# Optimization experiments

Hardware: AMD Instinct MI355X
Metric: run time of the kernel (lower is better)

Reference implementation:

```python
import jax, jax.numpy as jnp
import numpy as np


def gcn_conv(h, src, dst, n, W, b):
    # PyG GCNConv: linear, add self-loops, symmetric norm, scatter-sum, bias
    h = h @ W
    loop = jnp.arange(n)
    s = jnp.concatenate([src, loop])
    d = jnp.concatenate([dst, loop])
    deg = jax.ops.segment_sum(jnp.ones_like(d, h.dtype), d, num_segments=n)
    dinv = jnp.where(deg > 0, jax.lax.rsqrt(deg), 0.0)
    norm = dinv[s] * dinv[d]  # [E+N]
    out = jax.ops.segment_sum(h[s] * norm[:, None], d, num_segments=n)
    return out + b


def setup_inputs() -> dict:
    key = jax.random.key(0)
    ks = jax.random.split(key, 4)
    N, E, F_IN, F_H, F_OUT = 10000, 320000, 512, 128, 40
    x = jax.random.normal(ks[0], (N, F_IN), dtype=jnp.float32)
    edge_index = jax.random.randint(ks[1], (2, E), 0, N, dtype=jnp.int64)
    W1 = jax.random.normal(ks[2], (F_IN, F_H), dtype=jnp.float32) * (1.0 / np.sqrt(F_IN))
    b1 = jnp.zeros((F_H,), jnp.float32)
    W2 = jax.random.normal(ks[3], (F_H, F_OUT), dtype=jnp.float32) * (1.0 / np.sqrt(F_H))
    b2 = jnp.zeros((F_OUT,), jnp.float32)
    return {"x": x, "edge_index": edge_index, "W1": W1, "b1": b1, "W2": W2, "b2": b2}


def reference(x, edge_index, W1, b1, W2, b2):
    n = x.shape[0]
    src, dst = edge_index[0], edge_index[1]
    h = jax.nn.relu(gcn_conv(x, src, dst, n, W1, b1))
    logits = gcn_conv(h, src, dst, n, W2, b2)
    # regularizer: dense adjacency from edge list (duplicates summed), trace(L @ L)
    A = jnp.zeros((n, n), jnp.float32).at[src, dst].add(1.0)
    reg_loss = jnp.sum(A * A.T)  # == trace(A @ A)
    return jax.nn.log_softmax(logits, axis=1), reg_loss
```

## Files before the change

### kernel.cpp

```cpp
#include <hip/hip_runtime.h>
#include <hip/hip_bf16.h>


#define CAP 128

typedef __attribute__((ext_vector_type(8))) short short8;
typedef __attribute__((ext_vector_type(4))) float float4v;

__device__ __forceinline__ unsigned short f2bf(float f) {
    __hip_bfloat16 b = __float2bfloat16(f);
    return *reinterpret_cast<unsigned short*>(&b);
}
__device__ __forceinline__ float bf2f(unsigned short u) {
    __hip_bfloat16 b = *reinterpret_cast<__hip_bfloat16*>(&u);
    return __bfloat162float(b);
}

__global__ void k_prep(const float* __restrict__ W1, unsigned short* __restrict__ Bh1,
                       unsigned short* __restrict__ Bl1,
                       const float* __restrict__ W2, unsigned short* __restrict__ Bh2,
                       unsigned short* __restrict__ Bl2,
                       int* __restrict__ zbase, int zints, int p1B, int p2B) {
    int b = blockIdx.x;
    if (b < p1B) {
        int t = b * 256 + threadIdx.x;
        int lane = t & 63;
        int f = (t >> 6) % 8;
        int kb = (t >> 6) / 8;
        int kbase = kb * 32 + (lane >> 4) * 8;
        int n = f * 16 + (lane & 15);
        unsigned short hj[8], lj[8];
#pragma unroll
        for (int j = 0; j < 8; j++) {
            float v = W1[(size_t)(kbase + j) * 128 + n];
            unsigned short hb = f2bf(v);
            hj[j] = hb;
            lj[j] = f2bf(v - bf2f(hb));
        }
        ushort4 h0 = {hj[0], hj[1], hj[2], hj[3]}, h1 = {hj[4], hj[5], hj[6], hj[7]};
        ushort4 l0 = {lj[0], lj[1], lj[2], lj[3]}, l1 = {lj[4], lj[5], lj[6], lj[7]};
        ((ushort4*)Bh1)[t * 2] = h0; ((ushort4*)Bh1)[t * 2 + 1] = h1;
        ((ushort4*)Bl1)[t * 2] = l0; ((ushort4*)Bl1)[t * 2 + 1] = l1;
        return;
    }
    b -= p1B;
    if (b < p2B) {
        int t = b * 256 + threadIdx.x;
        if (t >= 4 * 3 * 64) return;
        int lane = t & 63;
        int f = (t >> 6) % 3;
        int kb = (t >> 6) / 3;
        int kbase = kb * 32 + (lane >> 4) * 8;
        int n = f * 16 + (lane & 15);
        unsigned short hj[8], lj[8];
#pragma unroll
        for (int j = 0; j < 8; j++) {
            float v = (n < 40) ? W2[(size_t)(kbase + j) * 40 + n] : 0.f;
            unsigned short hb = f2bf(v);
            hj[j] = hb;
            lj[j] = f2bf(v - bf2f(hb));
        }
        ushort4 h0 = {hj[0], hj[1], hj[2], hj[3]}, h1 = {hj[4], hj[5], hj[6], hj[7]};
        ushort4 l0 = {lj[0], lj[1], lj[2], lj[3]}, l1 = {lj[4], lj[5], lj[6], lj[7]};
        ((ushort4*)Bh2)[t * 2] = h0; ((ushort4*)Bh2)[t * 2 + 1] = h1;
        ((ushort4*)Bl2)[t * 2] = l0; ((ushort4*)Bl2)[t * 2 + 1] = l1;
        return;
    }
    b -= p2B;
    {
        int i = b * 256 + threadIdx.x;
        if (i < zints) zbase[i] = 0;
    }
}

__global__ void k_conv_fill(const float* __restrict__ x, unsigned short* __restrict__ xh,
                            int total4,
                            const int* __restrict__ src, const int* __restrict__ dst, int E,
                            int* __restrict__ cnt, unsigned short* __restrict__ csr,
                            int convB) {
    if ((int)blockIdx.x < convB) {
        int i = blockIdx.x * 256 + threadIdx.x;
        if (i < total4) {
            float4 v = ((const float4*)x)[i];
            ushort4 h;
            h.x = f2bf(v.x); h.y = f2bf(v.y); h.z = f2bf(v.z); h.w = f2bf(v.w);
            ((ushort4*)xh)[i] = h;
        }
        return;
    }
    int e = ((int)blockIdx.x - convB) * 256 + (int)threadIdx.x;
    if (e >= E) return;
    int d = dst[e];
    int pos = atomicAdd(&cnt[d], 1);
    if (pos < CAP) csr[(size_t)d * CAP + pos] = (unsigned short)src[e];
}

template <int NF, int KB>
__global__ void k_gemm1(const unsigned short* __restrict__ Xh,
                        const unsigned short* __restrict__ Bh,
                        const unsigned short* __restrict__ Bl,
                        unsigned short* __restrict__ H0, int M,
                        const int* __restrict__ cnt) {
    const int K = KB * 32, N = NF * 16;
    const int CH = NF * 64;
    __shared__ uint4 sB[2][2 * NF * 64];
    int w = threadIdx.x >> 6, lane = threadIdx.x & 63;
    int m0 = blockIdx.x * 32 + w * 16;
    bool valid = (m0 < M);
    int arow = valid ? (m0 + (lane & 15)) : 0;

    const uint4* GH = (const uint4*)Bh;
    const uint4* GL = (const uint4*)Bl;
    float4v acc[NF] = {};
    const short8* A = (const short8*)(Xh + (size_t)arow * K) + (lane >> 4);
    short8 a = A[0];

#pragma unroll
    for (int c = threadIdx.x; c < CH; c += 128) {
        sB[0][c] = GH[c];
        sB[0][CH + c] = GL[c];
    }
    __syncthreads();

    for (int kb = 0; kb < KB; kb++) {
        int slot = kb & 1;
        if (kb + 1 < KB) {
            const uint4* gh = GH + (kb + 1) * CH;
            const uint4* gl = GL + (kb + 1) * CH;
#pragma unroll
            for (int c = threadIdx.x; c < CH; c += 128) {
                sB[slot ^ 1][c] = gh[c];
                sB[slot ^ 1][CH + c] = gl[c];
            }
        }
        short8 an = (kb + 1 < KB) ? A[(kb + 1) * 4] : a;
        const short8* sb = (const short8*)sB[slot];
#pragma unroll
        for (int f = 0; f < NF; f++) {
            short8 bh = sb[f * 64 + lane];
            short8 bl = sb[CH + f * 64 + lane];
            acc[f] = __builtin_amdgcn_mfma_f32_16x16x32_bf16(a, bh, acc[f], 0, 0, 0);
            acc[f] = __builtin_amdgcn_mfma_f32_16x16x32_bf16(a, bl, acc[f], 0, 0, 0);
        }
        a = an;
        __syncthreads();
    }
    if (!valid) return;
    int row = (lane >> 4) * 4, col = lane & 15;
    float dd[4];
#pragma unroll
    for (int r = 0; r < 4; r++)
        dd[r] = rsqrtf((float)min(cnt[m0 + row + r], CAP) + 1.0f);
#pragma unroll
    for (int f = 0; f < NF; f++)
#pragma unroll
        for (int r = 0; r < 4; r++)
            H0[(size_t)(m0 + row + r) * N + f * 16 + col] = f2bf(acc[f][r] * dd[r]);
}

template <int NF, int KB>
__global__ void k_mfma_gemm2(const unsigned short* __restrict__ Ab,
                             const unsigned short* __restrict__ Bh,
                             const unsigned short* __restrict__ Bl,
                             unsigned short* __restrict__ LGb, int M,
                             const int* __restrict__ cnt) {
    const int K = KB * 32, N = NF * 16;
    const int TOT = KB * NF * 64;
    __shared__ uint4 sB[2 * KB * NF * 64];
#pragma unroll
    for (int c = threadIdx.x; c < TOT; c += 256) {
        sB[c] = ((const uint4*)Bh)[c];
        sB[TOT + c] = ((const uint4*)Bl)[c];
    }
    __syncthreads();
    int w = threadIdx.x >> 6, lane = threadIdx.x & 63;
    int m0 = blockIdx.x * 64 + w * 16;
    if (m0 >= M) return;
    float4v acc[NF] = {};
    const short8* A = (const short8*)(Ab + (size_t)(m0 + (lane & 15)) * K) + (lane >> 4);
    const short8* sb = (const short8*)sB;
#pragma unroll
    for (int kb = 0; kb < KB; kb++) {
        short8 a = A[kb * 4];
#pragma unroll
        for (int f = 0; f < NF; f++) {
            short8 bh = sb[(kb * NF + f) * 64 + lane];
            short8 bl = sb[TOT + (kb * NF + f) * 64 + lane];
            acc[f] = __builtin_amdgcn_mfma_f32_16x16x32_bf16(a, bh, acc[f], 0, 0, 0);
            acc[f] = __builtin_amdgcn_mfma_f32_16x16x32_bf16(a, bl, acc[f], 0, 0, 0);
        }
    }
    int row = (lane >> 4) * 4, col = lane & 15;
    float dd[4];
#pragma unroll
    for (int r = 0; r < 4; r++)
        dd[r] = rsqrtf((float)min(cnt[m0 + row + r], CAP) + 1.0f);
#pragma unroll
    for (int f = 0; f < NF; f++)
#pragma unroll
        for (int r = 0; r < 4; r++)
            LGb[(size_t)(m0 + row + r) * N + f * 16 + col] = f2bf(acc[f][r] * dd[r]);
}

__global__ void k_agg1_reg(const int* __restrict__ cnt, const unsigned short* __restrict__ csr,
                           const unsigned short* __restrict__ H, const float* __restrict__ b1,
                           unsigned* __restrict__ aggb,
                           const int* __restrict__ src, const int* __restrict__ dst, int E,
                           float* __restrict__ regp, int Nn, int aggBlocks) {
    if ((int)blockIdx.x < aggBlocks) {
        int wid = blockIdx.x * 4 + (threadIdx.x >> 6);
        int lane = threadIdx.x & 63;
        if (wid >= Nn) return;
        int len = min(cnt[wid], CAP);
        const unsigned* H2 = (const unsigned*)H;
        unsigned ph = H2[(unsigned)(wid << 6) + lane];
        float accx = __uint_as_float(ph << 16);
        float accy = __uint_as_float(ph & 0xffff0000u);
        const unsigned short* row = csr + (size_t)wid * CAP;
        int j = 0;
        for (; j + 16 <= len; j += 16) {
            uint4 iv0 = *(const uint4*)(row + j);
            uint4 iv1 = *(const uint4*)(row + j + 8);
            unsigned s[16];
            s[0] = iv0.x & 0xffff; s[1] = iv0.x >> 16; s[2] = iv0.y & 0xffff; s[3] = iv0.y >> 16;
            s[4] = iv0.z & 0xffff; s[5] = iv0.z >> 16; s[6] = iv0.w & 0xffff; s[7] = iv0.w >> 16;
            s[8] = iv1.x & 0xffff; s[9] = iv1.x >> 16; s[10] = iv1.y & 0xffff; s[11] = iv1.y >> 16;
            s[12] = iv1.z & 0xffff; s[13] = iv1.z >> 16; s[14] = iv1.w & 0xffff; s[15] = iv1.w >> 16;
            unsigned p[16];
#pragma unroll
            for (int q = 0; q < 16; q++) p[q] = H2[(s[q] << 6) + lane];
#pragma unroll
            for (int q = 0; q < 16; q++) {
                accx += __uint_as_float(p[q] << 16);
                accy += __uint_as_float(p[q] & 0xffff0000u);
            }
        }
        for (; j + 8 <= len; j += 8) {
            uint4 iv0 = *(const uint4*)(row + j);
            unsigned s[8];
            s[0] = iv0.x & 0xffff; s[1] = iv0.x >> 16; s[2] = iv0.y & 0xffff; s[3] = iv0.y >> 16;
            s[4] = iv0.z & 0xffff; s[5] = iv0.z >> 16; s[6] = iv0.w & 0xffff; s[7] = iv0.w >> 16;
            unsigned p[8];
#pragma unroll
            for (int q = 0; q < 8; q++) p[q] = H2[(s[q] << 6) + lane];
#pragma unroll
            for (int q = 0; q < 8; q++) {
                accx += __uint_as_float(p[q] << 16);
                accy += __uint_as_float(p[q] & 0xffff0000u);
            }
        }
        for (; j < len; j++) {
            unsigned p0 = H2[((unsigned)row[j] << 6) + lane];
            accx += __uint_as_float(p0 << 16);
            accy += __uint_as_float(p0 & 0xffff0000u);
        }
        float dd = rsqrtf((float)len + 1.0f);
        float2 bb = ((const float2*)b1)[lane];
        float vx = dd * accx + bb.x, vy = dd * accy + bb.y;
        vx = vx > 0.f ? vx : 0.f;
        vy = vy > 0.f ? vy : 0.f;
        aggb[(unsigned)(wid << 6) + lane] = (unsigned)f2bf(vx) | ((unsigned)f2bf(vy) << 16);
    } else {
        int e = ((int)blockIdx.x - aggBlocks) * 256 + (int)threadIdx.x;
        int c = 0;
        if (e < E) {
            int s = src[e];
            unsigned d = (unsigned)dst[e];
            int len = min(cnt[s], CAP);
            const unsigned short* row = csr + (size_t)s * CAP;
            for (int i = 0; i < len; i += 8) {
                uint4 v = *(const uint4*)(row + i);
                c += ((v.x & 0xffffu) == d) ? 1 : 0;
                c += ((v.x >> 16) == d && i + 1 < len) ? 1 : 0;
                c += ((v.y & 0xffffu) == d && i + 2 < len) ? 1 : 0;
                c += ((v.y >> 16) == d && i + 3 < len) ? 1 : 0;
                c += ((v.z & 0xffffu) == d && i + 4 < len) ? 1 : 0;
                c += ((v.z >> 16) == d && i + 5 < len) ? 1 : 0;
                c += ((v.w & 0xffffu) == d && i + 6 < len) ? 1 : 0;
                c += ((v.w >> 16) == d && i + 7 < len) ? 1 : 0;
            }
        }
#pragma unroll
        for (int off = 32; off; off >>= 1) c += __shfl_xor(c, off, 64);
        if ((threadIdx.x & 63) == 0 && c) atomicAdd(regp, (float)c);
    }
}

__global__ void k_agg2_lsm(const int* __restrict__ cnt, const unsigned short* __restrict__ csr,
                           const unsigned short* __restrict__ LGb, const float* __restrict__ b2,
                           const float* __restrict__ regp, float* __restrict__ out,
                           int Nn, int F) {
    int wid = (blockIdx.x * blockDim.x + threadIdx.x) >> 6;
    int lane = threadIdx.x & 63;
    if (wid >= Nn) return;
    int len = min(cnt[wid], CAP);
    bool act = lane < F;
    unsigned base = (unsigned)wid * 48 + lane;
    float acc = act ? bf2f(LGb[base]) : 0.f;
    const unsigned short* row = csr + (size_t)wid * CAP;
    int j = 0;
    for (; j + 8 <= len; j += 8) {
        uint4 idv = *(const uint4*)(row + j);
        unsigned s[8];
        s[0] = idv.x & 0xffff; s[1] = idv.x >> 16; s[2] = idv.y & 0xffff; s[3] = idv.y >> 16;
        s[4] = idv.z & 0xffff; s[5] = idv.z >> 16; s[6] = idv.w & 0xffff; s[7] = idv.w >> 16;
        unsigned short a[8];
#pragma unroll
        for (int q = 0; q < 8; q++) a[q] = act ? LGb[s[q] * 48 + lane] : (unsigned short)0;
#pragma unroll
        for (int q = 0; q < 8; q++) acc += __uint_as_float((unsigned)a[q] << 16);
    }
    for (; j < len; j++) {
        unsigned short a0 = act ? LGb[(unsigned)row[j] * 48 + lane] : (unsigned short)0;
        acc += __uint_as_float((unsigned)a0 << 16);
    }
    float dd = rsqrtf((float)len + 1.0f);
    float v = act ? dd * acc + b2[lane] : -1e30f;
    float m = v;
#pragma unroll
    for (int off = 32; off; off >>= 1) m = fmaxf(m, __shfl_xor(m, off, 64));
    float ex = act ? expf(v - m) : 0.f;
    float ssum = ex;
#pragma unroll
    for (int off = 32; off; off >>= 1) ssum += __shfl_xor(ssum, off, 64);
    if (act) out[(size_t)wid * F + lane] = v - m - logf(ssum);
    if (wid == 0 && lane == 0) out[(size_t)Nn * F] = regp[0];
}

extern "C" void kernel_launch(void* const* d_in, const int* in_sizes, int n_in,
                              void* d_out, int out_size, void* d_ws, size_t ws_size,
                              hipStream_t stream) {
    const float* x  = (const float*)d_in[0];
    const int*   ei = (const int*)d_in[1];
    const float* W1 = (const float*)d_in[2];
    const float* b1 = (const float*)d_in[3];
    const float* W2 = (const float*)d_in[4];
    const float* b2 = (const float*)d_in[5];
    float* out = (float*)d_out;

    const int FH   = in_sizes[3];
    const int FOUT = in_sizes[5];
    const int FIN  = in_sizes[2] / FH;
    const int Nn   = in_sizes[0] / FIN;
    const int E    = in_sizes[1] / 2;
    const int* src = ei;
    const int* dst = ei + E;

    int*   cnt  = (int*)d_ws;
    float* regp = (float*)(cnt + Nn);
    unsigned short* csr   = (unsigned short*)(regp + 16);
    unsigned short* Xh    = csr + (size_t)Nn * CAP;
    unsigned short* H0b   = Xh + (size_t)Nn * FIN;
    unsigned short* AGG1b = H0b + (size_t)Nn * FH;
    unsigned short* Bh1   = AGG1b + (size_t)Nn * FH;
    unsigned short* Bl1   = Bh1 + 65536;
    unsigned short* Bh2   = Bl1 + 65536;
    unsigned short* Bl2   = Bh2 + 6144;
    unsigned short* LGb   = Bl2 + 6144;

    int p1B = (16 * 8 * 64) / 256;
    int p2B = (4 * 3 * 64 + 255) / 256;
    int zints = Nn + 16;
    int zB = (zints + 255) / 256;
    k_prep<<<p1B + p2B + zB, 256, 0, stream>>>(W1, Bh1, Bl1, W2, Bh2, Bl2,
                                               cnt, zints, p1B, p2B);

    int total4 = Nn * FIN / 4;
    int convB = (total4 + 255) / 256;
    int fillB = (E + 255) / 256;
    k_conv_fill<<<convB + fillB, 256, 0, stream>>>(x, Xh, total4, src, dst, E, cnt, csr, convB);

    k_gemm1<8, 16><<<(Nn + 31) / 32, 128, 0, stream>>>(Xh, Bh1, Bl1, H0b, Nn, cnt);

    int aggBlocks = (Nn + 3) / 4;
    int regBlocks = (E + 255) / 256;
    k_agg1_reg<<<aggBlocks + regBlocks, 256, 0, stream>>>(
        cnt, csr, H0b, b1, (unsigned*)AGG1b, src, dst, E, regp, Nn, aggBlocks);

    k_mfma_gemm2<3, 4><<<(Nn + 63) / 64, 256, 0, stream>>>(AGG1b, Bh2, Bl2, LGb, Nn, cnt);

    k_agg2_lsm<<<(Nn * 64 + 255) / 256, 256, 0, stream>>>(
        cnt, csr, LGb, b2, regp, out, Nn, FOUT);
}
```

Measured before the change: 194.2 us.

## Move regularizer count into GEMM1 launch and split it across four lanes

The trace(A·A^T) edge-count work moves out of the aggregation kernel and into extra blocks of the first GEMM launch, so it can overlap with the compute-bound matmul instead of the memory-bound gather. The count loop is also restructured: four threads now scan each edge's CSR row with strided 8-element chunks, which shortens per-thread serial loops and balances load. Aggregation becomes a standalone kernel. The risk is that the extra blocks contend with GEMM blocks for CUs and may delay the GEMM tail.

```diff
diff --git a/kernel.cpp b/kernel.cpp
--- a/kernel.cpp
+++ b/kernel.cpp
@@ -96,11 +96,45 @@
 }
 
 template <int NF, int KB>
-__global__ void k_gemm1(const unsigned short* __restrict__ Xh,
-                        const unsigned short* __restrict__ Bh,
-                        const unsigned short* __restrict__ Bl,
-                        unsigned short* __restrict__ H0, int M,
-                        const int* __restrict__ cnt) {
+__global__ void k_gemm1_reg(const unsigned short* __restrict__ Xh,
+                            const unsigned short* __restrict__ Bh,
+                            const unsigned short* __restrict__ Bl,
+                            unsigned short* __restrict__ H0, int M,
+                            const int* __restrict__ cnt,
+                            const int* __restrict__ src, const int* __restrict__ dst, int E,
+                            const unsigned short* __restrict__ csr,
+                            float* __restrict__ regp, int gemmBlocks) {
+    if ((int)blockIdx.x >= gemmBlocks) {
+        int b = (int)blockIdx.x - gemmBlocks;
+        int g = threadIdx.x >> 2;
+        int sub = threadIdx.x & 3;
+        int base = b * 512;
+        int c = 0;
+        for (int it = 0; it < 16; it++) {
+            int e = base + it * 32 + g;
+            if (e < E) {
+                int s = src[e];
+                unsigned d = (unsigned)dst[e];
+                int len = min(cnt[s], CAP);
+                const unsigned short* row = csr + (size_t)s * CAP;
+                for (int i = sub * 8; i < len; i += 32) {
+                    uint4 v = *(const uint4*)(row + i);
+                    c += ((v.x & 0xffffu) == d) ? 1 : 0;
+                    c += ((v.x >> 16) == d && i + 1 < len) ? 1 : 0;
+                    c += ((v.y & 0xffffu) == d && i + 2 < len) ? 1 : 0;
+                    c += ((v.y >> 16) == d && i + 3 < len) ? 1 : 0;
+                    c += ((v.z & 0xffffu) == d && i + 4 < len) ? 1 : 0;
+                    c += ((v.z >> 16) == d && i + 5 < len) ? 1 : 0;
+                    c += ((v.w & 0xffffu) == d && i + 6 < len) ? 1 : 0;
+                    c += ((v.w >> 16) == d && i + 7 < len) ? 1 : 0;
+                }
+            }
+        }
+#pragma unroll
+        for (int off = 32; off; off >>= 1) c += __shfl_xor(c, off, 64);
+        if ((threadIdx.x & 63) == 0 && c) atomicAdd(regp, (float)c);
+        return;
+    }
     const int K = KB * 32, N = NF * 16;
     const int CH = NF * 64;
     __shared__ uint4 sB[2][2 * NF * 64];
@@ -156,6 +190,63 @@
 #pragma unroll
         for (int r = 0; r < 4; r++)
             H0[(size_t)(m0 + row + r) * N + f * 16 + col] = f2bf(acc[f][r] * dd[r]);
+}
+
+__global__ void k_agg1(const int* __restrict__ cnt, const unsigned short* __restrict__ csr,
+                       const unsigned short* __restrict__ H, const float* __restrict__ b1,
+                       unsigned* __restrict__ aggb, int Nn) {
+    int wid = (int)(blockIdx.x * blockDim.x + threadIdx.x) >> 6;
+    int lane = threadIdx.x & 63;
+    if (wid >= Nn) return;
+    int len = min(cnt[wid], CAP);
+    const unsigned* H2 = (const unsigned*)H;
+    unsigned ph = H2[(unsigned)(wid << 6) + lane];
+    float accx = __uint_as_float(ph << 16);
+    float accy = __uint_as_float(ph & 0xffff0000u);
+    const unsigned short* row = csr + (size_t)wid * CAP;
+    int j = 0;
+    for (; j + 16 <= len; j += 16) {
+        uint4 iv0 = *(const uint4*)(row + j);
+        uint4 iv1 = *(const uint4*)(row + j + 8);
+        unsigned s[16];
+        s[0] = iv0.x & 0xffff; s[1] = iv0.x >> 16; s[2] = iv0.y & 0xffff; s[3] = iv0.y >> 16;
+        s[4] = iv0.z & 0xffff; s[5] = iv0.z >> 16; s[6] = iv0.w & 0xffff; s[7] = iv0.w >> 16;
+        s[8] = iv1.x & 0xffff; s[9] = iv1.x >> 16; s[10] = iv1.y & 0xffff; s[11] = iv1.y >> 16;
+        s[12] = iv1.z & 0xffff; s[13] = iv1.z >> 16; s[14] = iv1.w & 0xffff; s[15] = iv1.w >> 16;
+        unsigned p[16];
+#pragma unroll
+        for (int q = 0; q < 16; q++) p[q] = H2[(s[q] << 6) + lane];
+#pragma unroll
+        for (int q = 0; q < 16; q++) {
+            accx += __uint_as_float(p[q] << 16);
+            accy += __uint_as_float(p[q] & 0xffff0000u);
+        }
+    }
+    for (; j + 8 <= len; j += 8) {
+        uint4 iv0 = *(const uint4*)(row + j);
+        unsigned s[8];
+        s[0] = iv0.x & 0xffff; s[1] = iv0.x >> 16; s[2] = iv0.y & 0xffff; s[3] = iv0.y >> 16;
+        s[4] = iv0.z & 0xffff; s[5] = iv0.z >> 16; s[6] = iv0.w & 0xffff; s[7] = iv0.w >> 16;
+        unsigned p[8];
+#pragma unroll
+        for (int q = 0; q < 8; q++) p[q] = H2[(s[q] << 6) + lane];
+#pragma unroll
+        for (int q = 0; q < 8; q++) {
+            accx += __uint_as_float(p[q] << 16);
+            accy += __uint_as_float(p[q] & 0xffff0000u);
+        }
+    }
+    for (; j < len; j++) {
+        unsigned p0 = H2[((unsigned)row[j] << 6) + lane];
+        accx += __uint_as_float(p0 << 16);
+        accy += __uint_as_float(p0 & 0xffff0000u);
+    }
+    float dd = rsqrtf((float)len + 1.0f);
+    float2 bb = ((const float2*)b1)[lane];
+    float vx = dd * accx + bb.x, vy = dd * accy + bb.y;
+    vx = vx > 0.f ? vx : 0.f;
+    vy = vy > 0.f ? vy : 0.f;
+    aggb[(unsigned)(wid << 6) + lane] = (unsigned)f2bf(vx) | ((unsigned)f2bf(vy) << 16);
 }
 
 template <int NF, int KB>
@@ -202,101 +293,16 @@
             LGb[(size_t)(m0 + row + r) * N + f * 16 + col] = f2bf(acc[f][r] * dd[r]);
 }
 
-__global__ void k_agg1_reg(const int* __restrict__ cnt, const unsigned short* __restrict__ csr,
-                           const unsigned short* __restrict__ H, const float* __restrict__ b1,
-                           unsigned* __restrict__ aggb,
-                           const int* __restrict__ src, const int* __restrict__ dst, int E,
-                           float* __restrict__ regp, int Nn, int aggBlocks) {
-    if ((int)blockIdx.x < aggBlocks) {
-        int wid = blockIdx.x * 4 + (threadIdx.x >> 6);
-        int lane = threadIdx.x & 63;
-        if (wid >= Nn) return;
-        int len = min(cnt[wid], CAP);
-        const unsigned* H2 = (const unsigned*)H;
-        unsigned ph = H2[(unsigned)(wid << 6) + lane];
-        float accx = __uint_as_float(ph << 16);
-        float accy = __uint_as_float(ph & 0xffff0000u);
-        const unsigned short* row = csr + (size_t)wid * CAP;
-        int j = 0;
-        for (; j + 16 <= len; j += 16) {
-            uint4 iv0 = *(const uint4*)(row + j);
-            uint4 iv1 = *(const uint4*)(row + j + 8);
-            unsigned s[16];
-            s[0] = iv0.x & 0xffff; s[1] = iv0.x >> 16; s[2] = iv0.y & 0xffff; s[3] = iv0.y >> 16;
-            s[4] = iv0.z & 0xffff; s[5] = iv0.z >> 16; s[6] = iv0.w & 0xffff; s[7] = iv0.w >> 16;
-            s[8] = iv1.x & 0xffff; s[9] = iv1.x >> 16; s[10] = iv1.y & 0xffff; s[11] = iv1.y >> 16;
-            s[12] = iv1.z & 0xffff; s[13] = iv1.z >> 16; s[14] = iv1.w & 0xffff; s[15] = iv1.w >> 16;
-            unsigned p[16];
-#pragma unroll
-            for (int q = 0; q < 16; q++) p[q] = H2[(s[q] << 6) + lane];
-#pragma unroll
-            for (int q = 0; q < 16; q++) {
-                accx += __uint_as_float(p[q] << 16);
-                accy += __uint_as_float(p[q] & 0xffff0000u);
-            }
-        }
-        for (; j + 8 <= len; j += 8) {
-            uint4 iv0 = *(const uint4*)(row + j);
-            unsigned s[8];
-            s[0] = iv0.x & 0xffff; s[1] = iv0.x >> 16; s[2] = iv0.y & 0xffff; s[3] = iv0.y >> 16;
-            s[4] = iv0.z & 0xffff; s[5] = iv0.z >> 16; s[6] = iv0.w & 0xffff; s[7] = iv0.w >> 16;
-            unsigned p[8];
-#pragma unroll
-            for (int q = 0; q < 8; q++) p[q] = H2[(s[q] << 6) + lane];
-#pragma unroll
-            for (int q = 0; q < 8; q++) {
-                accx += __uint_as_float(p[q] << 16);
-                accy += __uint_as_float(p[q] & 0xffff0000u);
-            }
-        }
-        for (; j < len; j++) {
-            unsigned p0 = H2[((unsigned)row[j] << 6) + lane];
-            accx += __uint_as_float(p0 << 16);
-            accy += __uint_as_float(p0 & 0xffff0000u);
-        }
-        float dd = rsqrtf((float)len + 1.0f);
-        float2 bb = ((const float2*)b1)[lane];
-        float vx = dd * accx + bb.x, vy = dd * accy + bb.y;
-        vx = vx > 0.f ? vx : 0.f;
-        vy = vy > 0.f ? vy : 0.f;
-        aggb[(unsigned)(wid << 6) + lane] = (unsigned)f2bf(vx) | ((unsigned)f2bf(vy) << 16);
-    } else {
-        int e = ((int)blockIdx.x - aggBlocks) * 256 + (int)threadIdx.x;
-        int c = 0;
-        if (e < E) {
-            int s = src[e];
-            unsigned d = (unsigned)dst[e];
-            int len = min(cnt[s], CAP);
-            const unsigned short* row = csr + (size_t)s * CAP;
-            for (int i = 0; i < len; i += 8) {
-                uint4 v = *(const uint4*)(row + i);
-                c += ((v.x & 0xffffu) == d) ? 1 : 0;
-                c += ((v.x >> 16) == d && i + 1 < len) ? 1 : 0;
-                c += ((v.y & 0xffffu) == d && i + 2 < len) ? 1 : 0;
-                c += ((v.y >> 16) == d && i + 3 < len) ? 1 : 0;
-                c += ((v.z & 0xffffu) == d && i + 4 < len) ? 1 : 0;
-                c += ((v.z >> 16) == d && i + 5 < len) ? 1 : 0;
-                c += ((v.w & 0xffffu) == d && i + 6 < len) ? 1 : 0;
-                c += ((v.w >> 16) == d && i + 7 < len) ? 1 : 0;
-            }
-        }
-#pragma unroll
-        for (int off = 32; off; off >>= 1) c += __shfl_xor(c, off, 64);
-        if ((threadIdx.x & 63) == 0 && c) atomicAdd(regp, (float)c);
-    }
-}
-
 __global__ void k_agg2_lsm(const int* __restrict__ cnt, const unsigned short* __restrict__ csr,
                            const unsigned short* __restrict__ LGb, const float* __restrict__ b2,
                            const float* __restrict__ regp, float* __restrict__ out,
                            int Nn, int F) {
-    int wid = (blockIdx.x * blockDim.x + threadIdx.x) >> 6;
+    int wid = (int)(blockIdx.x * blockDim.x + threadIdx.x) >> 6;
     int lane = threadIdx.x & 63;
     if (wid >= Nn) return;
     int len = min(cnt[wid], CAP);
     bool act = lane < F;
-    unsigned base = (unsigned)wid * 48 + lane;
-    float acc = act ? bf2f(LGb[base]) : 0.f;
+    float acc = act ? bf2f(LGb[(unsigned)wid * 48 + lane]) : 0.f;
     const unsigned short* row = csr + (size_t)wid * CAP;
     int j = 0;
     for (; j + 8 <= len; j += 8) {
@@ -370,12 +376,12 @@
     int fillB = (E + 255) / 256;
     k_conv_fill<<<convB + fillB, 256, 0, stream>>>(x, Xh, total4, src, dst, E, cnt, csr, convB);
 
-    k_gemm1<8, 16><<<(Nn + 31) / 32, 128, 0, stream>>>(Xh, Bh1, Bl1, H0b, Nn, cnt);
-
-    int aggBlocks = (Nn + 3) / 4;
-    int regBlocks = (E + 255) / 256;
-    k_agg1_reg<<<aggBlocks + regBlocks, 256, 0, stream>>>(
-        cnt, csr, H0b, b1, (unsigned*)AGG1b, src, dst, E, regp, Nn, aggBlocks);
+    int gemmB = (Nn + 31) / 32;
+    int regB  = (E + 511) / 512;
+    k_gemm1_reg<8, 16><<<gemmB + regB, 128, 0, stream>>>(
+        Xh, Bh1, Bl1, H0b, Nn, cnt, src, dst, E, csr, regp, gemmB);
+
+    k_agg1<<<(Nn * 64 + 255) / 256, 256, 0, stream>>>(cnt, csr, H0b, b1, (unsigned*)AGG1b, Nn);
 
     k_mfma_gemm2<3, 4><<<(Nn + 63) / 64, 256, 0, stream>>>(AGG1b, Bh2, Bl2, LGb, Nn, cnt);
 
```

Result: faster. 169.9 us (-12.5%).
